# Optimization experiments

Hardware: AMD Instinct MI355X
Metric: run time of the kernel (lower is better)

Reference implementation:

```python
import jax, jax.numpy as jnp
import numpy as np
from math import sqrt

EMA_W = 0.3  # ema_weight
LN_EPS = 1e-5


def setup_inputs() -> dict:
    key = jax.random.key(0)
    ks = jax.random.split(key, 16)
    B, L, H, E = 8, 1024, 8, 64
    d_ff, dp_rank = 2048, 8
    inp = {
        "queries": jax.random.normal(ks[0], (B, L, H, E), jnp.float32),
        "keys": jax.random.normal(ks[1], (B, L, H, E), jnp.float32),
        "values": jax.random.normal(ks[2], (B, L, H, E), jnp.float32),
        "attn_mask": jnp.zeros((B, 1, L, L), jnp.bool_),
        # dynamic-projection mlp: Linear(E, dp_rank)
        "mlp_w": jax.random.normal(ks[3], (E, dp_rank), jnp.float32) / sqrt(E),
        "mlp_b": jnp.zeros((dp_rank,), jnp.float32),
        # ff_1: Linear(E,d_ff) -> GELU -> Linear(d_ff,E)
        "ff1_w1": jax.random.normal(ks[4], (E, d_ff), jnp.float32) / sqrt(E),
        "ff1_b1": jnp.zeros((d_ff,), jnp.float32),
        "ff1_w2": jax.random.normal(ks[5], (d_ff, E), jnp.float32) / sqrt(d_ff),
        "ff1_b2": jnp.zeros((E,), jnp.float32),
        # ff_2
        "ff2_w1": jax.random.normal(ks[6], (E, d_ff), jnp.float32) / sqrt(E),
        "ff2_b1": jnp.zeros((d_ff,), jnp.float32),
        "ff2_w2": jax.random.normal(ks[7], (d_ff, E), jnp.float32) / sqrt(d_ff),
        "ff2_b2": jnp.zeros((E,), jnp.float32),
        # LayerNorm(E)
        "ln_w": jnp.ones((E,), jnp.float32),
        "ln_b": jnp.zeros((E,), jnp.float32),
    }
    return inp


def _dynamic_projection(src, mlp_w, mlp_b):
    # src: [B,L,H,E] -> softmax over dp_rank, then einsum 'blhe,blhr->blhe'
    sm = jax.nn.softmax(src @ mlp_w + mlp_b, axis=-1)  # [B,L,H,R]
    return jnp.einsum('blhe,blhr->blhe', src, sm)


def _ffn(x, w1, b1, w2, b2):
    return jax.nn.gelu(x @ w1 + b1, approximate=False) @ w2 + b2


def reference(queries, keys, values, attn_mask,
              mlp_w, mlp_b,
              ff1_w1, ff1_b1, ff1_w2, ff1_b2,
              ff2_w1, ff2_b1, ff2_w2, ff2_b2,
              ln_w, ln_b):
    E = queries.shape[-1]
    scale = 1.0 / sqrt(24.0)   # hardcoded in source
    scale1 = 1.0 / sqrt(E)

    dp_values = _dynamic_projection(values, mlp_w, mlp_b)
    dp_keys = _dynamic_projection(keys, mlp_w, mlp_b)

    # ema state starts at zeros every forward, so ema = (1-w) * x
    ema_queries = (1.0 - EMA_W) * queries
    ema_keys = (1.0 - EMA_W) * dp_keys

    # NOTE: source masks a scores tensor that is then overwritten; mask has
    # no effect on the output, so attn_mask is unused (kept for fidelity).
    scores = jnp.einsum('blhe,bshe->bhls', ema_queries, ema_keys)
    scores1 = jnp.einsum('blhe,bshe->bhls', queries, keys)

    A = jax.nn.softmax(scale * scores, axis=-1)    # dropout = identity (eval)
    A1 = jax.nn.softmax(scale1 * scores1, axis=-1)

    V = jnp.einsum('bhls,bshd->blhd', A, dp_values)
    V1 = jnp.einsum('bhls,bshd->blhd', A1, values)

    src = _ffn(V, ff1_w1, ff1_b1, ff1_w2, ff1_b2) + _ffn(V1, ff2_w1, ff2_b1, ff2_w2, ff2_b2)

    mu = jnp.mean(src, axis=-1, keepdims=True)
    var = jnp.mean(jnp.square(src - mu), axis=-1, keepdims=True)
    out = (src - mu) * jax.lax.rsqrt(var + LN_EPS) * ln_w + ln_b
    return out
```

## Files before the change

### kernel.cpp

```cpp
#include <hip/hip_runtime.h>

typedef _Float16 f16x8 __attribute__((ext_vector_type(8)));
typedef _Float16 f16x2 __attribute__((ext_vector_type(2)));
typedef float f32x4 __attribute__((ext_vector_type(4)));
typedef float f32x16 __attribute__((ext_vector_type(16)));
typedef unsigned short u16x8 __attribute__((ext_vector_type(8)));
typedef unsigned int u32x4 __attribute__((ext_vector_type(4)));

static __device__ __forceinline__ unsigned short f2h(float x) {
  return __builtin_bit_cast(unsigned short, (_Float16)x);
}
static __device__ __forceinline__ float h2f(unsigned short u) {
  return (float)__builtin_bit_cast(_Float16, u);
}

static __device__ __forceinline__ f16x2 gelu_pk(f16x2 x) {
  const f16x2 P4 = {(_Float16)4.0f, (_Float16)4.0f};
  const f16x2 N4 = {(_Float16)-4.0f, (_Float16)-4.0f};
  const f16x2 C1 = {(_Float16)0.392761f, (_Float16)0.392761f};
  const f16x2 C3 = {(_Float16)-0.0512736f, (_Float16)-0.0512736f};
  const f16x2 C5 = {(_Float16)0.00376322f, (_Float16)0.00376322f};
  const f16x2 C7 = {(_Float16)-0.000100287f, (_Float16)-0.000100287f};
  const f16x2 HF = {(_Float16)0.5f, (_Float16)0.5f};
  const f16x2 ONE = {(_Float16)1.0f, (_Float16)1.0f};
  const f16x2 ZRO = {(_Float16)0.0f, (_Float16)0.0f};
  f16x2 xc = __builtin_elementwise_max(__builtin_elementwise_min(x, P4), N4);
  f16x2 u = xc * xc;
  f16x2 p = __builtin_elementwise_fma(
      __builtin_elementwise_fma(__builtin_elementwise_fma(C7, u, C5), u, C3),
      u, C1);
  f16x2 q = __builtin_elementwise_fma(xc, p, HF);
  f16x2 qc = __builtin_elementwise_max(__builtin_elementwise_min(q, ONE), ZRO);
  return x * qc;
}

static __device__ __forceinline__ int sig16(int v) {
  return (v & ~12) | ((v & 4) << 1) | ((v & 8) >> 1);
}

__global__ __launch_bounds__(256) void k_prep(
    const float* __restrict__ vsrc, const float* __restrict__ ksrc,
    const float* __restrict__ w11, const float* __restrict__ w21,
    const float* __restrict__ w12, const float* __restrict__ w22,
    unsigned short* __restrict__ vtb, unsigned short* __restrict__ kf16,
    unsigned short* __restrict__ w1t1, unsigned short* __restrict__ w2t1,
    unsigned short* __restrict__ w1t2, unsigned short* __restrict__ w2t2) {
  int bid = blockIdx.x, tid = threadIdx.x;
  if (bid >= 1152) {
    int kb = bid - 1152, bh = kb >> 4, lt = kb & 15, b = bh >> 3, h = bh & 7;
    const float* src = ksrc + (((b * 1024 + lt * 64) * 8 + h) << 6);
    unsigned short* dst = kf16 + bh * 65536 + lt * 64 * 64;
#pragma unroll
    for (int i = 0; i < 2; ++i) {
      int c = tid + i * 256, r = c >> 3, c0 = (c & 7) * 8;
      const float* s = src + r * 512 + c0;
      f32x4 a = *(const f32x4*)s, b4 = *(const f32x4*)(s + 4);
      u16x8 vv;
#pragma unroll
      for (int j = 0; j < 4; ++j) { vv[j] = f2h(a[j]); vv[j + 4] = f2h(b4[j]); }
      *(u16x8*)(dst + r * 64 + c0) = vv;
    }
    return;
  }
  __shared__ unsigned short t[64][72];
  const float* src; unsigned short* dst; int srs, drs;
  bool isw2 = false;
  if (bid < 1024) {
    int bh = bid >> 4, lt = bid & 15, b = bh >> 3, h = bh & 7;
    src = vsrc + (((b * 1024 + lt * 64) * 8 + h) << 6); srs = 512;
    dst = vtb + bh * 65536 + lt * 64; drs = 1024;
  } else {
    int wb = bid - 1024, which = wb >> 5, ti = wb & 31;
    isw2 = (which & 1);
    if (which == 0)      { src = w11 + ti * 64;   srs = 2048; dst = w1t1 + ti * 4096; drs = 64; }
    else if (which == 1) { src = w21 + ti * 4096; srs = 64;   dst = w2t1 + ti * 64;   drs = 2048; }
    else if (which == 2) { src = w12 + ti * 64;   srs = 2048; dst = w1t2 + ti * 4096; drs = 64; }
    else                 { src = w22 + ti * 4096; srs = 64;   dst = w2t2 + ti * 64;   drs = 2048; }
  }
#pragma unroll
  for (int i = 0; i < 2; ++i) {
    int c = tid + i * 256, r = c >> 3, c0 = (c & 7) * 8;
    const float* s = src + r * srs + c0;
    int tr = isw2 ? sig16(r) : r;
#pragma unroll
    for (int j = 0; j < 8; ++j) t[c0 + j][tr] = f2h(s[j]);
  }
  __syncthreads();
#pragma unroll
  for (int i = 0; i < 2; ++i) {
    int c = tid + i * 256, r = c >> 3, c0 = (c & 7) * 8;
    u16x8 vv;
#pragma unroll
    for (int j = 0; j < 8; ++j) vv[j] = t[r][c0 + j];
    *(u16x8*)(dst + r * drs + c0) = vv;
  }
}

__global__ __launch_bounds__(64) __attribute__((amdgpu_waves_per_eu(1, 1)))
void k_attn(
    const float* __restrict__ q, const unsigned short* __restrict__ kf16,
    const unsigned short* __restrict__ vtb,
    unsigned short* __restrict__ Vo, unsigned short* __restrict__ V1o) {
  int bid = blockIdx.x;
  int swz = (bid & 7) * 512 + (bid >> 3);
  int bh = swz >> 6, rem = swz & 63, qt = rem >> 2, w = rem & 3;
  int b = bh >> 3, h = bh & 7;
  int lane = threadIdx.x & 63, t = lane & 15, g = lane >> 4;

  __shared__ unsigned short Pl[2][1024];

  f16x8 aq[2];
  {
    int row = qt * 64 + w * 16 + t;
    const float* qp = q + ((b * 1024 + row) * 8 + h) * 64;
#pragma unroll
    for (int ks = 0; ks < 2; ++ks) {
      f32x4 q0 = *(const f32x4*)(qp + ks * 32 + g * 8);
      f32x4 q1 = *(const f32x4*)(qp + ks * 32 + g * 8 + 4);
      f16x8 a;
#pragma unroll
      for (int j = 0; j < 4; ++j) { a[j] = (_Float16)q0[j]; a[j + 4] = (_Float16)q1[j]; }
      aq[ks] = a;
    }
  }

  const float scl[2] = {0.14429954f, 0.18033688f};
  float lsp[2][4];
  f32x4 o[2][4];
#pragma unroll
  for (int i = 0; i < 4; ++i) {
    lsp[0][i] = 0.f; lsp[1][i] = 0.f;
    o[0][i] = (f32x4){0, 0, 0, 0}; o[1][i] = (f32x4){0, 0, 0, 0};
  }

  const unsigned short* kfb = kf16 + bh * 65536;
  const unsigned short* vbase = vtb + bh * 65536;

  f16x8 bk[8];
#pragma unroll
  for (int ks = 0; ks < 2; ++ks)
#pragma unroll
    for (int nt = 0; nt < 4; ++nt)
      bk[ks * 4 + nt] = *(const f16x8*)(kfb + (nt * 16 + t) * 64 + (ks * 4 + g) * 8);

#pragma unroll 1
  for (int kt = 0; kt < 16; ++kt) {
    f16x8 bv[8];
#pragma unroll
    for (int ks = 0; ks < 2; ++ks)
#pragma unroll
      for (int nt = 0; nt < 4; ++nt)
        bv[ks * 4 + nt] = *(const f16x8*)(vbase + (nt * 16 + t) * 1024 + kt * 64 + (ks * 4 + g) * 8);

    f32x4 s[4];
#pragma unroll
    for (int nt = 0; nt < 4; ++nt) s[nt] = (f32x4){0, 0, 0, 0};
#pragma unroll
    for (int ks = 0; ks < 2; ++ks)
#pragma unroll
      for (int nt = 0; nt < 4; ++nt)
        s[nt] = __builtin_amdgcn_mfma_f32_16x16x32_f16(aq[ks], bk[ks * 4 + nt], s[nt], 0, 0, 0);

    if (kt < 15) {
#pragma unroll
      for (int ks = 0; ks < 2; ++ks)
#pragma unroll
        for (int nt = 0; nt < 4; ++nt)
          bk[ks * 4 + nt] = *(const f16x8*)(kfb + ((kt + 1) * 64 + nt * 16 + t) * 64 + (ks * 4 + g) * 8);
    }
    __builtin_amdgcn_sched_barrier(0);

#pragma unroll
    for (int v = 0; v < 2; ++v) {
      float pr[4][4];
#pragma unroll
      for (int nt = 0; nt < 4; ++nt)
#pragma unroll
        for (int reg = 0; reg < 4; ++reg)
          pr[nt][reg] = fminf(exp2f(s[nt][reg] * scl[v]), 60000.0f);
#pragma unroll
      for (int nt = 0; nt < 4; ++nt)
#pragma unroll
        for (int reg = 0; reg < 4; ++reg) {
          int r = g * 4 + reg, sc = nt * 16 + t;
          Pl[v][r * 64 + ((((sc >> 3) ^ (r & 7)) << 3) | (sc & 7))] = f2h(pr[nt][reg]);
        }
#pragma unroll
      for (int reg = 0; reg < 4; ++reg)
        lsp[v][reg] += (pr[0][reg] + pr[1][reg]) + (pr[2][reg] + pr[3][reg]);
    }
    asm volatile("s_waitcnt lgkmcnt(0)" ::: "memory");
#pragma unroll
    for (int v = 0; v < 2; ++v)
#pragma unroll
      for (int ks = 0; ks < 2; ++ks) {
        f16x8 ap = *(const f16x8*)&Pl[v][t * 64 + (((ks * 4 + g) ^ (t & 7)) << 3)];
#pragma unroll
        for (int nt = 0; nt < 4; ++nt)
          o[v][nt] = __builtin_amdgcn_mfma_f32_16x16x32_f16(ap, bv[ks * 4 + nt], o[v][nt], 0, 0, 0);
      }
  }

#pragma unroll
  for (int v = 0; v < 2; ++v)
#pragma unroll
    for (int dd = 1; dd < 16; dd <<= 1)
#pragma unroll
      for (int reg = 0; reg < 4; ++reg)
        lsp[v][reg] += __shfl_xor(lsp[v][reg], dd);

#pragma unroll
  for (int nt = 0; nt < 4; ++nt)
#pragma unroll
    for (int reg = 0; reg < 4; ++reg) {
      int row = qt * 64 + w * 16 + g * 4 + reg;
      int idx = ((b * 1024 + row) * 8 + h) * 64 + nt * 16 + t;
      float r0 = __builtin_amdgcn_rcpf(lsp[0][reg]);
      float r1 = __builtin_amdgcn_rcpf(lsp[1][reg]);
      Vo[idx]  = f2h(o[0][nt][reg] * r0);
      V1o[idx] = f2h(o[1][nt][reg] * r1);
    }
}

static __device__ __forceinline__ void compute_chunk(
    int j, const unsigned short* __restrict__ W1buf,
    const unsigned short* __restrict__ W2buf,
    const float* __restrict__ biasL, const f16x8 (&bx)[4],
    f32x16& acc0, f32x16& acc1, int t5, int hh) {
  f32x16 d0, d1;
#pragma unroll
  for (int rq = 0; rq < 4; ++rq) {
    f32x4 bb0 = *(const f32x4*)(biasL + j * 64 + rq * 8 + hh * 4);
    f32x4 bb1 = *(const f32x4*)(biasL + j * 64 + 32 + rq * 8 + hh * 4);
#pragma unroll
    for (int jj = 0; jj < 4; ++jj) { d0[rq * 4 + jj] = bb0[jj]; d1[rq * 4 + jj] = bb1[jj]; }
  }
#pragma unroll
  for (int ks = 0; ks < 4; ++ks) {
    int fr0 = t5;
    f16x8 aw0 = *(const f16x8*)&W1buf[fr0 * 64 + (((ks * 2 + hh) ^ (fr0 & 7)) << 3)];
    d0 = __builtin_amdgcn_mfma_f32_32x32x16_f16(aw0, bx[ks], d0, 0, 0, 0);
    int fr1 = 32 + t5;
    f16x8 aw1 = *(const f16x8*)&W1buf[fr1 * 64 + (((ks * 2 + hh) ^ (fr1 & 7)) << 3)];
    d1 = __builtin_amdgcn_mfma_f32_32x32x16_f16(aw1, bx[ks], d1, 0, 0, 0);
  }
#pragma unroll
  for (int g = 0; g < 4; ++g) {
    u32x4 av;
#pragma unroll
    for (int q = 0; q < 4; ++q) {
      int base = (g & 1) * 8 + 2 * q;
      float lo = (g < 2) ? d0[base] : d1[base];
      float hi = (g < 2) ? d0[base + 1] : d1[base + 1];
      f16x2 hx = __builtin_bit_cast(f16x2, __builtin_amdgcn_cvt_pkrtz(lo, hi));
      av[q] = __builtin_bit_cast(unsigned, gelu_pk(hx));
    }
    f16x8 hb = __builtin_bit_cast(f16x8, av);
    int er0 = t5;
    f16x8 wa0 = *(const f16x8*)&W2buf[er0 * 64 + (((g * 2 + hh) ^ (er0 & 7)) << 3)];
    acc0 = __builtin_amdgcn_mfma_f32_32x32x16_f16(wa0, hb, acc0, 0, 0, 0);
    int er1 = 32 + t5;
    f16x8 wa1 = *(const f16x8*)&W2buf[er1 * 64 + (((g * 2 + hh) ^ (er1 & 7)) << 3)];
    acc1 = __builtin_amdgcn_mfma_f32_32x32x16_f16(wa1, hb, acc1, 0, 0, 0);
  }
}

__global__ __launch_bounds__(256) void k_ffn(
    const unsigned short* __restrict__ Vo, const unsigned short* __restrict__ V1o,
    const unsigned short* __restrict__ w1ta, const unsigned short* __restrict__ w2ta,
    const unsigned short* __restrict__ w1tb, const unsigned short* __restrict__ w2tb,
    const float* __restrict__ b1a, const float* __restrict__ b1b,
    unsigned short* __restrict__ p0, unsigned short* __restrict__ p1,
    unsigned short* __restrict__ p2, unsigned short* __restrict__ p3) {
  int bid = blockIdx.x;
  int quar = bid >> 9, rb = bid & 511;
  int tid = threadIdx.x, w = tid >> 6, lane = tid & 63;
  int t5 = lane & 31, hh = lane >> 5;
  int rowbase = rb * 128 + w * 32;
  unsigned short* pout = (quar == 0) ? p0 : (quar == 1) ? p1 : (quar == 2) ? p2 : p3;

  __shared__ unsigned short W1c[4096];
  __shared__ unsigned short W2c[4096];
  __shared__ float biasL[2][512];

  if (tid < 128) {
    *(f32x4*)&biasL[0][tid * 4] = *(const f32x4*)(b1a + quar * 512 + tid * 4);
    *(f32x4*)&biasL[1][tid * 4] = *(const f32x4*)(b1b + quar * 512 + tid * 4);
  }

  f32x16 acc0, acc1;
#pragma unroll
  for (int i = 0; i < 16; ++i) { acc0[i] = 0.f; acc1[i] = 0.f; }

  int r0 = tid >> 3, c8 = tid & 7;
  int sw = (c8 ^ (r0 & 7)) << 3;

#pragma unroll 1
  for (int ffn = 0; ffn < 2; ++ffn) {
    const unsigned short* X = ffn ? V1o : Vo;
    const unsigned short* w1t = ffn ? w1tb : w1ta;
    const unsigned short* w2t = ffn ? w2tb : w2ta;
    f16x8 bx[4];
#pragma unroll
    for (int ks = 0; ks < 4; ++ks)
      bx[ks] = *(const f16x8*)(X + (rowbase + t5) * 64 + ks * 16 + hh * 8);

    int cbase = quar * 8;
    u16x8 ra0 = *(const u16x8*)(w1t + (cbase * 64 + r0) * 64 + c8 * 8);
    u16x8 ra1 = *(const u16x8*)(w1t + (cbase * 64 + r0 + 32) * 64 + c8 * 8);
    u16x8 rb0 = *(const u16x8*)(w2t + r0 * 2048 + cbase * 64 + c8 * 8);
    u16x8 rb1 = *(const u16x8*)(w2t + (r0 + 32) * 2048 + cbase * 64 + c8 * 8);

#pragma unroll 1
    for (int j = 0; j < 8; ++j) {
      __syncthreads();
      *(u16x8*)&W1c[r0 * 64 + sw] = ra0;
      *(u16x8*)&W2c[r0 * 64 + sw] = rb0;
      *(u16x8*)&W1c[(r0 + 32) * 64 + sw] = ra1;
      *(u16x8*)&W2c[(r0 + 32) * 64 + sw] = rb1;
      __syncthreads();
      if (j < 7) {
        int c1 = cbase + j + 1;
        ra0 = *(const u16x8*)(w1t + (c1 * 64 + r0) * 64 + c8 * 8);
        ra1 = *(const u16x8*)(w1t + (c1 * 64 + r0 + 32) * 64 + c8 * 8);
        rb0 = *(const u16x8*)(w2t + r0 * 2048 + c1 * 64 + c8 * 8);
        rb1 = *(const u16x8*)(w2t + (r0 + 32) * 2048 + c1 * 64 + c8 * 8);
      }
      compute_chunk(j, W1c, W2c, &biasL[ffn][0], bx, acc0, acc1, t5, hh);
    }
  }

  int orow = rowbase + t5;
#pragma unroll
  for (int q = 0; q < 8; ++q) {
    int e0 = (2 * q & 3) + 8 * (q >> 1) + 4 * hh;
    unsigned pa = __builtin_bit_cast(unsigned,
        __builtin_amdgcn_cvt_pkrtz(acc0[2 * q], acc0[2 * q + 1]));
    unsigned pb = __builtin_bit_cast(unsigned,
        __builtin_amdgcn_cvt_pkrtz(acc1[2 * q], acc1[2 * q + 1]));
    *(unsigned*)(pout + orow * 64 + e0) = pa;
    *(unsigned*)(pout + orow * 64 + 32 + e0) = pb;
  }
}

__global__ __launch_bounds__(256) void k_reduce(
    const unsigned short* __restrict__ p0, const unsigned short* __restrict__ p1,
    const unsigned short* __restrict__ p2, const unsigned short* __restrict__ p3,
    const float* __restrict__ b2a, const float* __restrict__ b2b,
    const float* __restrict__ lnw, const float* __restrict__ lnb,
    float* __restrict__ out) {
  int tid = threadIdx.x, w = tid >> 6, lane = tid & 63;
  float bias = b2a[lane] + b2b[lane];
  float lw = lnw[lane], lb = lnb[lane];
  int wid = blockIdx.x * 4 + w;
#pragma unroll 4
  for (int i = 0; i < 16; ++i) {
    int r = wid * 16 + i;
    int ix = r * 64 + lane;
    float v = (h2f(p0[ix]) + h2f(p1[ix])) + (h2f(p2[ix]) + h2f(p3[ix])) + bias;
    float s1 = v, s2 = v * v;
#pragma unroll
    for (int dd = 1; dd < 64; dd <<= 1) {
      s1 += __shfl_xor(s1, dd);
      s2 += __shfl_xor(s2, dd);
    }
    float mu = s1 * 0.015625f;
    float var = s2 * 0.015625f - mu * mu;
    out[ix] = (v - mu) * rsqrtf(var + 1e-5f) * lw + lb;
  }
}

extern "C" void kernel_launch(void* const* d_in, const int* in_sizes, int n_in,
                              void* d_out, int out_size, void* d_ws, size_t ws_size,
                              hipStream_t stream) {
  (void)in_sizes; (void)n_in; (void)out_size; (void)ws_size;
  const float* q   = (const float*)d_in[0];
  const float* k   = (const float*)d_in[1];
  const float* v   = (const float*)d_in[2];
  const float* w11 = (const float*)d_in[6];
  const float* b11 = (const float*)d_in[7];
  const float* w21 = (const float*)d_in[8];
  const float* b21 = (const float*)d_in[9];
  const float* w12 = (const float*)d_in[10];
  const float* b12 = (const float*)d_in[11];
  const float* w22 = (const float*)d_in[12];
  const float* b22 = (const float*)d_in[13];
  const float* lnw = (const float*)d_in[14];
  const float* lnb = (const float*)d_in[15];

  unsigned short* vtb  = (unsigned short*)d_ws;
  unsigned short* Vo   = vtb + 4194304;
  unsigned short* V1o  = Vo + 4194304;
  unsigned short* w1t1 = V1o + 4194304;
  unsigned short* w2t1 = w1t1 + 131072;
  unsigned short* w1t2 = w2t1 + 131072;
  unsigned short* w2t2 = w1t2 + 131072;
  unsigned short* part1 = w2t2 + 131072;
  unsigned short* kf16  = part1 + 4194304;
  unsigned short* part3 = kf16 + 4194304;
  unsigned short* part0 = vtb;
  unsigned short* part2 = kf16;

  k_prep<<<dim3(2176), dim3(256), 0, stream>>>(v, k, w11, w21, w12, w22,
                                               vtb, kf16, w1t1, w2t1, w1t2, w2t2);
  k_attn<<<dim3(4096), dim3(64), 0, stream>>>(q, kf16, vtb, Vo, V1o);
  k_ffn<<<dim3(2048), dim3(256), 0, stream>>>(Vo, V1o, w1t1, w2t1, w1t2, w2t2,
                                              b11, b12, part0, part1, part2, part3);
  k_reduce<<<dim3(1024), dim3(256), 0, stream>>>(part0, part1, part2, part3,
                                                 b21, b22, lnw, lnb, (float*)d_out);
}
```

Measured before the change: 248.5 us.

## Process two 16-row query subtiles per wave in attention kernel to reuse K/V loads

Each single-wave attention block now handles 32 query rows (two 16-row subtiles) instead of 16, so every K and V fragment loaded from global memory feeds twice as many MFMAs. The grid is halved, the block-index swizzle is adjusted, and the shared probability buffer is doubled. The aim is to halve K/V global traffic per query row and amortize load latency. In exchange, register pressure roughly doubles for accumulators and scores, the occupancy hint is relaxed to allow up to 2 waves per EU, and there are fewer blocks to spread across CUs.

```diff
diff --git a/kernel.cpp b/kernel.cpp
--- a/kernel.cpp
+++ b/kernel.cpp
@@ -96,22 +96,23 @@
   }
 }
 
-__global__ __launch_bounds__(64) __attribute__((amdgpu_waves_per_eu(1, 1)))
+__global__ __launch_bounds__(64) __attribute__((amdgpu_waves_per_eu(1, 2)))
 void k_attn(
     const float* __restrict__ q, const unsigned short* __restrict__ kf16,
     const unsigned short* __restrict__ vtb,
     unsigned short* __restrict__ Vo, unsigned short* __restrict__ V1o) {
   int bid = blockIdx.x;
-  int swz = (bid & 7) * 512 + (bid >> 3);
-  int bh = swz >> 6, rem = swz & 63, qt = rem >> 2, w = rem & 3;
+  int swz = (bid & 7) * 256 + (bid >> 3);
+  int bh = swz >> 5, rb = swz & 31;
   int b = bh >> 3, h = bh & 7;
   int lane = threadIdx.x & 63, t = lane & 15, g = lane >> 4;
 
-  __shared__ unsigned short Pl[2][1024];
-
-  f16x8 aq[2];
-  {
-    int row = qt * 64 + w * 16 + t;
+  __shared__ unsigned short Pl[2][2048];
+
+  f16x8 aq[2][2];
+#pragma unroll
+  for (int sub = 0; sub < 2; ++sub) {
+    int row = rb * 32 + sub * 16 + t;
     const float* qp = q + ((b * 1024 + row) * 8 + h) * 64;
 #pragma unroll
     for (int ks = 0; ks < 2; ++ks) {
@@ -120,18 +121,22 @@
       f16x8 a;
 #pragma unroll
       for (int j = 0; j < 4; ++j) { a[j] = (_Float16)q0[j]; a[j + 4] = (_Float16)q1[j]; }
-      aq[ks] = a;
+      aq[sub][ks] = a;
     }
   }
 
   const float scl[2] = {0.14429954f, 0.18033688f};
-  float lsp[2][4];
-  f32x4 o[2][4];
-#pragma unroll
-  for (int i = 0; i < 4; ++i) {
-    lsp[0][i] = 0.f; lsp[1][i] = 0.f;
-    o[0][i] = (f32x4){0, 0, 0, 0}; o[1][i] = (f32x4){0, 0, 0, 0};
-  }
+  float lsp[2][2][4];
+  f32x4 o[2][2][4];
+#pragma unroll
+  for (int v = 0; v < 2; ++v)
+#pragma unroll
+    for (int sub = 0; sub < 2; ++sub)
+#pragma unroll
+      for (int i = 0; i < 4; ++i) {
+        lsp[v][sub][i] = 0.f;
+        o[v][sub][i] = (f32x4){0, 0, 0, 0};
+      }
 
   const unsigned short* kfb = kf16 + bh * 65536;
   const unsigned short* vbase = vtb + bh * 65536;
@@ -152,14 +157,19 @@
       for (int nt = 0; nt < 4; ++nt)
         bv[ks * 4 + nt] = *(const f16x8*)(vbase + (nt * 16 + t) * 1024 + kt * 64 + (ks * 4 + g) * 8);
 
-    f32x4 s[4];
-#pragma unroll
-    for (int nt = 0; nt < 4; ++nt) s[nt] = (f32x4){0, 0, 0, 0};
+    f32x4 s[2][4];
+#pragma unroll
+    for (int sub = 0; sub < 2; ++sub)
+#pragma unroll
+      for (int nt = 0; nt < 4; ++nt) s[sub][nt] = (f32x4){0, 0, 0, 0};
 #pragma unroll
     for (int ks = 0; ks < 2; ++ks)
 #pragma unroll
-      for (int nt = 0; nt < 4; ++nt)
-        s[nt] = __builtin_amdgcn_mfma_f32_16x16x32_f16(aq[ks], bk[ks * 4 + nt], s[nt], 0, 0, 0);
+      for (int sub = 0; sub < 2; ++sub)
+#pragma unroll
+        for (int nt = 0; nt < 4; ++nt)
+          s[sub][nt] = __builtin_amdgcn_mfma_f32_16x16x32_f16(
+              aq[sub][ks], bk[ks * 4 + nt], s[sub][nt], 0, 0, 0);
 
     if (kt < 15) {
 #pragma unroll
@@ -171,55 +181,66 @@
     __builtin_amdgcn_sched_barrier(0);
 
 #pragma unroll
-    for (int v = 0; v < 2; ++v) {
-      float pr[4][4];
-#pragma unroll
-      for (int nt = 0; nt < 4; ++nt)
+    for (int v = 0; v < 2; ++v)
+#pragma unroll
+      for (int sub = 0; sub < 2; ++sub) {
+        float pr[4][4];
+#pragma unroll
+        for (int nt = 0; nt < 4; ++nt)
+#pragma unroll
+          for (int reg = 0; reg < 4; ++reg)
+            pr[nt][reg] = fminf(exp2f(s[sub][nt][reg] * scl[v]), 60000.0f);
+#pragma unroll
+        for (int nt = 0; nt < 4; ++nt)
+#pragma unroll
+          for (int reg = 0; reg < 4; ++reg) {
+            int r = g * 4 + reg, sc = nt * 16 + t;
+            Pl[v][(sub * 16 + r) * 64 + ((((sc >> 3) ^ (r & 7)) << 3) | (sc & 7))] =
+                f2h(pr[nt][reg]);
+          }
 #pragma unroll
         for (int reg = 0; reg < 4; ++reg)
-          pr[nt][reg] = fminf(exp2f(s[nt][reg] * scl[v]), 60000.0f);
-#pragma unroll
-      for (int nt = 0; nt < 4; ++nt)
-#pragma unroll
-        for (int reg = 0; reg < 4; ++reg) {
-          int r = g * 4 + reg, sc = nt * 16 + t;
-          Pl[v][r * 64 + ((((sc >> 3) ^ (r & 7)) << 3) | (sc & 7))] = f2h(pr[nt][reg]);
+          lsp[v][sub][reg] += (pr[0][reg] + pr[1][reg]) + (pr[2][reg] + pr[3][reg]);
+      }
+    asm volatile("s_waitcnt lgkmcnt(0)" ::: "memory");
+#pragma unroll
+    for (int v = 0; v < 2; ++v)
+#pragma unroll
+      for (int ks = 0; ks < 2; ++ks)
+#pragma unroll
+        for (int sub = 0; sub < 2; ++sub) {
+          f16x8 ap = *(const f16x8*)&Pl[v][(sub * 16 + t) * 64 +
+                                           (((ks * 4 + g) ^ (t & 7)) << 3)];
+#pragma unroll
+          for (int nt = 0; nt < 4; ++nt)
+            o[v][sub][nt] = __builtin_amdgcn_mfma_f32_16x16x32_f16(
+                ap, bv[ks * 4 + nt], o[v][sub][nt], 0, 0, 0);
         }
-#pragma unroll
-      for (int reg = 0; reg < 4; ++reg)
-        lsp[v][reg] += (pr[0][reg] + pr[1][reg]) + (pr[2][reg] + pr[3][reg]);
-    }
-    asm volatile("s_waitcnt lgkmcnt(0)" ::: "memory");
-#pragma unroll
-    for (int v = 0; v < 2; ++v)
-#pragma unroll
-      for (int ks = 0; ks < 2; ++ks) {
-        f16x8 ap = *(const f16x8*)&Pl[v][t * 64 + (((ks * 4 + g) ^ (t & 7)) << 3)];
-#pragma unroll
-        for (int nt = 0; nt < 4; ++nt)
-          o[v][nt] = __builtin_amdgcn_mfma_f32_16x16x32_f16(ap, bv[ks * 4 + nt], o[v][nt], 0, 0, 0);
+  }
+
+#pragma unroll
+  for (int v = 0; v < 2; ++v)
+#pragma unroll
+    for (int sub = 0; sub < 2; ++sub)
+#pragma unroll
+      for (int dd = 1; dd < 16; dd <<= 1)
+#pragma unroll
+        for (int reg = 0; reg < 4; ++reg)
+          lsp[v][sub][reg] += __shfl_xor(lsp[v][sub][reg], dd);
+
+#pragma unroll
+  for (int sub = 0; sub < 2; ++sub)
+#pragma unroll
+    for (int nt = 0; nt < 4; ++nt)
+#pragma unroll
+      for (int reg = 0; reg < 4; ++reg) {
+        int row = rb * 32 + sub * 16 + g * 4 + reg;
+        int idx = ((b * 1024 + row) * 8 + h) * 64 + nt * 16 + t;
+        float r0 = __builtin_amdgcn_rcpf(lsp[0][sub][reg]);
+        float r1 = __builtin_amdgcn_rcpf(lsp[1][sub][reg]);
+        Vo[idx]  = f2h(o[0][sub][nt][reg] * r0);
+        V1o[idx] = f2h(o[1][sub][nt][reg] * r1);
       }
-  }
-
-#pragma unroll
-  for (int v = 0; v < 2; ++v)
-#pragma unroll
-    for (int dd = 1; dd < 16; dd <<= 1)
-#pragma unroll
-      for (int reg = 0; reg < 4; ++reg)
-        lsp[v][reg] += __shfl_xor(lsp[v][reg], dd);
-
-#pragma unroll
-  for (int nt = 0; nt < 4; ++nt)
-#pragma unroll
-    for (int reg = 0; reg < 4; ++reg) {
-      int row = qt * 64 + w * 16 + g * 4 + reg;
-      int idx = ((b * 1024 + row) * 8 + h) * 64 + nt * 16 + t;
-      float r0 = __builtin_amdgcn_rcpf(lsp[0][reg]);
-      float r1 = __builtin_amdgcn_rcpf(lsp[1][reg]);
-      Vo[idx]  = f2h(o[0][nt][reg] * r0);
-      V1o[idx] = f2h(o[1][nt][reg] * r1);
-    }
 }
 
 static __device__ __forceinline__ void compute_chunk(
@@ -403,7 +424,7 @@
 
   k_prep<<<dim3(2176), dim3(256), 0, stream>>>(v, k, w11, w21, w12, w22,
                                                vtb, kf16, w1t1, w2t1, w1t2, w2t2);
-  k_attn<<<dim3(4096), dim3(64), 0, stream>>>(q, kf16, vtb, Vo, V1o);
+  k_attn<<<dim3(2048), dim3(64), 0, stream>>>(q, kf16, vtb, Vo, V1o);
   k_ffn<<<dim3(2048), dim3(256), 0, stream>>>(Vo, V1o, w1t1, w2t1, w1t2, w2t2,
                                               b11, b12, part0, part1, part2, part3);
   k_reduce<<<dim3(1024), dim3(256), 0, stream>>>(part0, part1, part2, part3,
```

After: 221.0 us. 1.12x faster.
